# Performance work log

Hardware: AMD Instinct MI355X
Metric: run time of the kernel (lower is better)

## Reference

```python
import jax, jax.numpy as jnp
import numpy as np

NUM_BINS = 36
EPS = 1e-12
BASE_DROP, MIN_DROP, MAX_DROP = 0.3, 0.1, 0.6
SENSITIVITY, NORMAL_APE = 4.0, 0.78


def _hann(n):
    # torch.hann_window default (periodic=True): 0.5*(1 - cos(2*pi*k/N))
    return 0.5 - 0.5 * jnp.cos(2.0 * jnp.pi * jnp.arange(n, dtype=jnp.float32) / n)


def compute_ape(images):
    B, C, H, W = images.shape
    mean = jnp.array([0.485, 0.456, 0.406], dtype=images.dtype).reshape(1, 3, 1, 1)
    std = jnp.array([0.229, 0.224, 0.225], dtype=images.dtype).reshape(1, 3, 1, 1)
    wts = jnp.array([0.2989, 0.587, 0.114], dtype=images.dtype).reshape(1, 3, 1, 1)
    gray = ((images * std + mean) * wts).sum(axis=1)  # (B,H,W)
    gray = gray - gray.mean(axis=(1, 2), keepdims=True)
    gray = gray * (_hann(H)[:, None] * _hann(W)[None, :])
    P = jnp.abs(jnp.fft.fft2(gray)) ** 2
    P = jnp.fft.fftshift(P, axes=(1, 2))
    cy, cx = (H - 1) / 2.0, (W - 1) / 2.0
    yy = jnp.arange(H, dtype=jnp.float32)[:, None] - cy
    xx = jnp.arange(W, dtype=jnp.float32)[None, :] - cx
    r = jnp.sqrt(xx ** 2 + yy ** 2)
    theta = (jnp.arctan2(yy, xx) + 2 * jnp.pi) % (2 * jnp.pi)
    r_max = r.max()
    radial_mask = (r >= 0.05 * r_max) & (r <= 0.95 * r_max)
    bin_width = 2 * jnp.pi / NUM_BINS
    idx = jnp.clip((theta / bin_width).astype(jnp.int32), 0, NUM_BINS - 1)  # (H,W)
    # batched masked angular histogram: one segment_sum over B*NUM_BINS segments
    Pm = (P * radial_mask).reshape(B, -1)
    seg = (idx.reshape(-1)[None, :] + NUM_BINS * jnp.arange(B)[:, None]).reshape(-1)
    energy = jax.ops.segment_sum(Pm.reshape(-1), seg, num_segments=B * NUM_BINS)
    energy = energy.reshape(B, NUM_BINS)
    total = energy.sum(axis=1, keepdims=True)
    p = energy / (total + EPS)
    H_theta = -(p * jnp.log(p + EPS)).sum(axis=1)
    ape = jnp.clip(H_theta / np.log(NUM_BINS), 0.0, 1.0)
    return jnp.where(total[:, 0] <= EPS, 0.0, ape)


def ape_to_dropout_prob(ape):
    adj = jnp.tanh((NORMAL_APE - ape) * SENSITIVITY)
    drop = jnp.where(adj >= 0,
                     BASE_DROP + adj * (MAX_DROP - BASE_DROP),
                     BASE_DROP + adj * (BASE_DROP - MIN_DROP))
    return jnp.clip(drop, MIN_DROP, MAX_DROP)


def adaptive_dropout(x, probs, key):
    # per-sample dropout: mask ~ Bernoulli(1-p), scale by 1/(1-p+1e-8)
    p = probs[:, None, None]
    keep = jax.random.bernoulli(key, 1.0 - p, x.shape).astype(x.dtype)
    out = x * keep / (1.0 - p + 1e-8)
    return jnp.where(p > 0, out, x)


def setup_inputs() -> dict:
    key = jax.random.key(0)
    k1, k2, k3, k4 = jax.random.split(key, 4)
    B, N, D, Hf = 64, 256, 768, 768
    images = jax.random.uniform(k1, (B, 3, 448, 448), dtype=jnp.float32)
    x = jax.random.normal(k2, (B, N, D), dtype=jnp.float32)
    w1 = jax.random.normal(k3, (Hf, D), dtype=jnp.float32) * (1.0 / np.sqrt(D))
    w2 = jax.random.normal(k4, (D, Hf), dtype=jnp.float32) * (1.0 / np.sqrt(Hf))
    return {"images": images, "x": x, "w1": w1, "w2": w2}


def reference(images, x, w1, w2):
    ape = compute_ape(images)
    probs = jax.lax.stop_gradient(ape_to_dropout_prob(ape))  # torch casts to python float -> detached
    k0, k1, k2 = jax.random.split(jax.random.key(1), 3)
    h = adaptive_dropout(x, probs, k0)            # input dropout
    h = jnp.einsum('bnd,hd->bnh', h, w1)          # fc1 (bias=False)
    h = jax.nn.gelu(h, approximate=False)         # nn.GELU (exact erf)
    h = adaptive_dropout(h, probs, k1)
    y = jnp.einsum('bnh,dh->bnd', h, w2)          # fc2 (bias=False)
    y = adaptive_dropout(y, probs, k2)
    return y
```

## Files before the change

kernel.cpp:

```cpp
#include <hip/hip_runtime.h>
#include <stdint.h>
#include <math.h>

typedef __attribute__((ext_vector_type(8))) short short8;
typedef __attribute__((ext_vector_type(4))) float floatx4;

#define IMGN 448
#define HW   200704
#define NBATCH 64
#define NBINS 36

#define MFMA(a, b, c) __builtin_amdgcn_mfma_f32_16x16x32_bf16((a), (b), (c), 0, 0, 0)

#define WAITBAR8() asm volatile("s_waitcnt vmcnt(8)\ns_barrier" ::: "memory")
#define WAITBAR6() asm volatile("s_waitcnt vmcnt(6)\ns_barrier" ::: "memory")
#define WAITBAR4() asm volatile("s_waitcnt vmcnt(4)\ns_barrier" ::: "memory")
#define WAITBAR0() asm volatile("s_waitcnt vmcnt(0)\ns_barrier" ::: "memory")
#define ENDBAR()   asm volatile("s_waitcnt lgkmcnt(0)\ns_barrier" ::: "memory")

#define WS_WIN   0u
#define WS_BINS  4096u
#define WS_TS    24576u
#define WS_BIDX  32768u
#define WS_TW    1048576u
#define TWSZ     401408u
#define WS_W     4194304u
#define WSZ      1179648u
#define WS_REG1  16777216u
#define GSZ      25690112u
#define CBSZ     13762560u
#define XSZ      25165824u
#define WS_REG2  75497472u

__host__ __device__ __forceinline__ uint32_t rotl32(uint32_t v, int r) {
  return (v << r) | (v >> (32 - r));
}
__host__ __device__ __forceinline__ void tf2x32(uint32_t k0, uint32_t k1,
                                                uint32_t x0, uint32_t x1,
                                                uint32_t &o0, uint32_t &o1) {
  uint32_t k2 = k0 ^ k1 ^ 0x1BD11BDAu;
  uint32_t v0 = x0 + k0, v1 = x1 + k1;
#define TFR(r) { v0 += v1; v1 = rotl32(v1, r); v1 ^= v0; }
  TFR(13) TFR(15) TFR(26) TFR(6)   v0 += k1; v1 += k2 + 1u;
  TFR(17) TFR(29) TFR(16) TFR(24)  v0 += k2; v1 += k0 + 2u;
  TFR(13) TFR(15) TFR(26) TFR(6)   v0 += k0; v1 += k1 + 3u;
  TFR(17) TFR(29) TFR(16) TFR(24)  v0 += k1; v1 += k2 + 4u;
  TFR(13) TFR(15) TFR(26) TFR(6)   v0 += k2; v1 += k0 + 5u;
#undef TFR
  o0 = v0; o1 = v1;
}
__device__ __forceinline__ float tf_uniform(uint32_t k0, uint32_t k1, uint32_t idx) {
  uint32_t a, b;
  tf2x32(k0, k1, 0u, idx, a, b);
  uint32_t bits = a ^ b;
  return __uint_as_float((bits >> 9) | 0x3F800000u) - 1.0f;
}

__device__ __forceinline__ unsigned short bf16rne(float v) {
  unsigned u = __float_as_uint(v);
  return (unsigned short)((u + 0x7fffu + ((u >> 16) & 1u)) >> 16);
}
__device__ __forceinline__ void split2(float v, unsigned short &h, unsigned short &l) {
  h = bf16rne(v);
  float fh = __uint_as_float(((unsigned)h) << 16);
  l = bf16rne(v - fh);
}

__device__ __forceinline__ void gload16(const void *g, void *l) {
  __builtin_amdgcn_global_load_lds(
      (const __attribute__((address_space(1))) unsigned int *)g,
      (__attribute__((address_space(3))) unsigned int *)l, 16, 0, 0);
}

__global__ __launch_bounds__(256) void k_prep(float *__restrict__ win,
                                              double *__restrict__ bins,
                                              uint8_t *__restrict__ bidx) {
  int t = blockIdx.x * 256 + threadIdx.x;
  int a = t / IMGN, b = t % IMGN;
  double yy = (double)((a + 224) % IMGN) - 223.5;
  double xx = (double)((b + 224) % IMGN) - 223.5;
  double r2 = xx * xx + yy * yy;
  uint8_t idx = 255;
  if (r2 >= 249.76125 && r2 <= 90163.81125) {
    double th = atan2(yy, xx);
    if (th < 0.0) th += 6.283185307179586476925286766559;
    int i = (int)(th / 0.17453292519943295769236907684886);
    if (i > 35) i = 35;
    if (i < 0) i = 0;
    idx = (uint8_t)i;
  }
  bidx[t] = idx;
  if (t < IMGN) {
    double ang = 6.283185307179586476925286766559 * (double)t / 448.0;
    win[t] = (float)(0.5 - 0.5 * cos(ang));
  }
  if (t < NBATCH * NBINS) bins[t] = 0.0;
}

__global__ __launch_bounds__(256) void k_tw(short8 *__restrict__ tch, short8 *__restrict__ tcl,
                                            short8 *__restrict__ tsh, short8 *__restrict__ tsl) {
  int wid = blockIdx.x * 256 + threadIdx.x;
  int lane = wid & 63;
  int tmp = wid >> 6;
  int kb = tmp % 14, mb = tmp / 14;
  int m = mb * 16 + (lane & 15);
  int k0 = kb * 32 + (lane >> 4) * 8;
  short8 ch, cl, sh, sl;
#pragma unroll
  for (int e = 0; e < 8; ++e) {
    int mm = (m * (k0 + e)) % IMGN;
    double ang = -6.283185307179586476925286766559 * (double)mm / 448.0;
    float c = (float)cos(ang), s = (float)sin(ang);
    unsigned short h, l;
    split2(c, h, l); ch[e] = (short)h; cl[e] = (short)l;
    split2(s, h, l); sh[e] = (short)h; sl[e] = (short)l;
  }
  tch[wid] = ch; tcl[wid] = cl; tsh[wid] = sh; tsl[wid] = sl;
}

__global__ __launch_bounds__(256) void k_wconv(const float *__restrict__ w1, const float *__restrict__ w2,
                                               short8 *__restrict__ w1h, short8 *__restrict__ w1l,
                                               short8 *__restrict__ w2h, short8 *__restrict__ w2l) {
  int wid = blockIdx.x * 256 + threadIdx.x;
  const float *src = blockIdx.y ? w2 : w1;
  short8 *dh = blockIdx.y ? w2h : w1h;
  short8 *dl = blockIdx.y ? w2l : w1l;
  int lane = wid & 63;
  int tmp = wid >> 6;
  int kb = tmp % 24, nb = tmp / 24;
  int n = nb * 16 + (lane & 15);
  int k0 = kb * 32 + (lane >> 4) * 8;
  const float *p = src + (size_t)n * 768 + k0;
  short8 vh, vl;
#pragma unroll
  for (int e = 0; e < 8; ++e) {
    unsigned short h, l;
    split2(p[e], h, l);
    vh[e] = (short)h; vl[e] = (short)l;
  }
  dh[wid] = vh; dl[wid] = vl;
}

__global__ __launch_bounds__(256) void k_gprep(const float *__restrict__ img, const float *__restrict__ win,
                                               short8 *__restrict__ gh, short8 *__restrict__ gl) {
  int wid = blockIdx.x * 256 + threadIdx.x;
  int lane = wid & 63;
  int tmp = wid >> 6;
  int kb = tmp % 14, nb = tmp / 14;
  int n = nb * 16 + (lane & 15);
  int b = n / 448, y = n % 448;
  int x0 = kb * 32 + (lane >> 4) * 8;
  const float *p = img + (size_t)b * 3 * HW + y * IMGN + x0;
  float wy = win[y];
  short8 vh, vl;
#pragma unroll
  for (int e = 0; e < 8; ++e) {
    float r = p[e], g = p[HW + e], bl = p[2 * HW + e];
    float t0 = (r * 0.229f + 0.485f) * 0.2989f;
    float t1 = (g * 0.224f + 0.456f) * 0.587f;
    float t2 = (bl * 0.225f + 0.406f) * 0.114f;
    float v = ((t0 + t1) + t2) * wy * win[x0 + e];
    unsigned short h, l;
    split2(v, h, l);
    vh[e] = (short)h; vl[e] = (short)l;
  }
  gh[wid] = vh; gl[wid] = vl;
}

__global__ __launch_bounds__(256) void k_rows(const short8 *__restrict__ tch, const short8 *__restrict__ tcl,
                                              const short8 *__restrict__ tsh, const short8 *__restrict__ tsl,
                                              const short8 *__restrict__ gh, const short8 *__restrict__ gl,
                                              short8 *__restrict__ crh, short8 *__restrict__ crl,
                                              short8 *__restrict__ cih, short8 *__restrict__ cil) {
  __shared__ short8 S[2][512];
  int orig = blockIdx.x;
  int swz = (orig & 7) * 224 + (orig >> 3);
  int mtg = swz & 3, ntg = swz >> 2;
  int tid = threadIdx.x;
  int lane = tid & 63, w = tid >> 6;
  int g = lane >> 4, c = lane & 15;
  int mt = mtg * 4 + w;
  floatx4 s_c[4] = {}, s_s[4] = {};
  short8 aAc, aAcl, aAs, aAsl, aBc, aBcl, aBs, aBsl;

#define R_STAGE(buf, kb) { \
  _Pragma("unroll") for (int i = 0; i < 2; ++i) { \
    int ch = w * 2 + i; \
    const short8 *m0 = (ch >> 2) ? gl : gh; \
    int row = ntg * 4 + (ch & 3); \
    gload16(m0 + ((size_t)row * 14 + (kb)) * 64 + lane, (char *)&S[buf][0] + ch * 1024); } }
#define R_LOADA(p, kb) { int ao = (mt * 14 + (kb)) * 64 + lane; \
  p##c = tch[ao]; p##cl = tcl[ao]; p##s = tsh[ao]; p##sl = tsl[ao]; }
#define R_COMPUTE(buf, p) { const short8 *Sc = &S[buf][0]; \
  _Pragma("unroll") for (int nt = 0; nt < 4; ++nt) { \
    short8 bh = Sc[nt * 64 + lane]; \
    short8 bl = Sc[(4 + nt) * 64 + lane]; \
    s_c[nt] = MFMA(p##c, bh, s_c[nt]); \
    s_c[nt] = MFMA(p##c, bl, s_c[nt]); \
    s_c[nt] = MFMA(p##cl, bh, s_c[nt]); \
    s_s[nt] = MFMA(p##s, bh, s_s[nt]); \
    s_s[nt] = MFMA(p##s, bl, s_s[nt]); \
    s_s[nt] = MFMA(p##sl, bh, s_s[nt]); } }

  R_STAGE(0, 0); R_LOADA(aA, 0);
  for (int kb = 0; kb < 14; kb += 2) {
    R_STAGE(1, kb + 1); R_LOADA(aB, kb + 1);
    WAITBAR6();
    R_COMPUTE(0, aA);
    ENDBAR();
    if (kb < 12) { R_STAGE(0, kb + 2); R_LOADA(aA, kb + 2); WAITBAR6(); }
    else { WAITBAR0(); }
    R_COMPUTE(1, aB);
    ENDBAR();
  }
#pragma unroll
  for (int nt = 0; nt < 4; ++nt) {
    int nrow = (ntg * 4 + nt) * 16 + c;
    int b = nrow / 448, y = nrow % 448;
    int kb2 = y >> 5;
    int lofs = 16 * ((y & 31) >> 3);
    int e2 = y & 7;
#pragma unroll
    for (int r = 0; r < 4; ++r) {
      int v = mt * 16 + 4 * g + r;
      if (v < 240) {
        int n2 = b * 240 + v;
        size_t word = ((size_t)(n2 >> 4) * 14 + kb2) * 64 + (n2 & 15) + lofs;
        unsigned short h, l;
        split2(s_c[nt][r], h, l);
        ((unsigned short *)crh)[word * 8 + e2] = h;
        ((unsigned short *)crl)[word * 8 + e2] = l;
        split2(s_s[nt][r], h, l);
        ((unsigned short *)cih)[word * 8 + e2] = h;
        ((unsigned short *)cil)[word * 8 + e2] = l;
      }
    }
  }
}

__global__ __launch_bounds__(256) void k_cols(const short8 *__restrict__ tch, const short8 *__restrict__ tcl,
                                              const short8 *__restrict__ tsh, const short8 *__restrict__ tsl,
                                              const short8 *__restrict__ crh, const short8 *__restrict__ crl,
                                              const short8 *__restrict__ cih, const short8 *__restrict__ cil,
                                              const uint8_t *__restrict__ bidx, double *__restrict__ bins) {
  __shared__ short8 S[2][1024];
  __shared__ double lb[72];
  int orig = blockIdx.x;
  int swz = (orig & 7) * 210 + (orig >> 3);
  int mtg = swz % 7, ntg = swz / 7;
  int tid = threadIdx.x;
  if (tid < 72) lb[tid] = 0.0;
  int lane = tid & 63, w = tid >> 6;
  int g = lane >> 4, c = lane & 15;
  int mt = mtg * 4 + w;
  int nt0 = ntg * 4;
  floatx4 s_cc[4] = {}, s_sc[4] = {}, s_ss[4] = {}, s_cs[4] = {};
  short8 aAc, aAcl, aAs, aAsl, aBc, aBcl, aBs, aBsl;

#define C_STAGE(buf, kb) { \
  _Pragma("unroll") for (int i = 0; i < 4; ++i) { \
    int ch = w * 4 + i; int sel = ch >> 2; \
    const short8 *m0 = sel == 0 ? crh : sel == 1 ? crl : sel == 2 ? cih : cil; \
    int row = nt0 + (ch & 3); \
    gload16(m0 + ((size_t)row * 14 + (kb)) * 64 + lane, (char *)&S[buf][0] + ch * 1024); } }
#define C_LOADA(p, kb) { int ao = (mt * 14 + (kb)) * 64 + lane; \
  p##c = tch[ao]; p##cl = tcl[ao]; p##s = tsh[ao]; p##sl = tsl[ao]; }
#define C_COMPUTE(buf, p) { const short8 *Sc = &S[buf][0]; \
  _Pragma("unroll") for (int nt = 0; nt < 4; ++nt) { \
    short8 brh = Sc[nt * 64 + lane]; \
    short8 brl = Sc[(4 + nt) * 64 + lane]; \
    short8 bih = Sc[(8 + nt) * 64 + lane]; \
    short8 bil = Sc[(12 + nt) * 64 + lane]; \
    s_cc[nt] = MFMA(p##c, brh, s_cc[nt]); \
    s_cc[nt] = MFMA(p##c, brl, s_cc[nt]); \
    s_cc[nt] = MFMA(p##cl, brh, s_cc[nt]); \
    s_sc[nt] = MFMA(p##s, brh, s_sc[nt]); \
    s_sc[nt] = MFMA(p##s, brl, s_sc[nt]); \
    s_sc[nt] = MFMA(p##sl, brh, s_sc[nt]); \
    s_ss[nt] = MFMA(p##s, bih, s_ss[nt]); \
    s_ss[nt] = MFMA(p##s, bil, s_ss[nt]); \
    s_ss[nt] = MFMA(p##sl, bih, s_ss[nt]); \
    s_cs[nt] = MFMA(p##c, bih, s_cs[nt]); \
    s_cs[nt] = MFMA(p##c, bil, s_cs[nt]); \
    s_cs[nt] = MFMA(p##cl, bih, s_cs[nt]); } }

  C_STAGE(0, 0); C_LOADA(aA, 0);
  for (int kb = 0; kb < 14; kb += 2) {
    C_STAGE(1, kb + 1); C_LOADA(aB, kb + 1);
    WAITBAR8();
    C_COMPUTE(0, aA);
    ENDBAR();
    if (kb < 12) { C_STAGE(0, kb + 2); C_LOADA(aA, kb + 2); WAITBAR8(); }
    else { WAITBAR0(); }
    C_COMPUTE(1, aB);
    ENDBAR();
  }
  int base_b = (ntg * 64) / 240;
  int cb0 = -1, cb1 = -1, cb2 = -1, cb3 = -1;
  double cv0 = 0.0, cv1 = 0.0, cv2 = 0.0, cv3 = 0.0;
#define PUTBIN(slot_, val_)                                                    \
  { int _s = (slot_); double _v = (val_);                                      \
    if (_s == cb0) cv0 += _v;                                                  \
    else if (_s == cb1) cv1 += _v;                                             \
    else if (_s == cb2) cv2 += _v;                                             \
    else if (_s == cb3) cv3 += _v;                                             \
    else {                                                                     \
      if (cb3 >= 0) atomicAdd(&lb[cb3], cv3);                                  \
      cb3 = cb2; cv3 = cv2; cb2 = cb1; cv2 = cv1;                              \
      cb1 = cb0; cv1 = cv0; cb0 = _s; cv0 = _v;                                \
    } }
#pragma unroll
  for (int nt = 0; nt < 4; ++nt) {
    int n = (nt0 + nt) * 16 + c;
    int v = n % 240;
    int bloc = n / 240 - base_b;
    if (v < 225) {
#pragma unroll
      for (int r = 0; r < 4; ++r) {
        int u = mt * 16 + 4 * g + r;
        float frv = s_cc[nt][r] - s_ss[nt][r];
        float fiv = s_sc[nt][r] + s_cs[nt][r];
        double P = (double)frv * frv + (double)fiv * fiv;
        int i1 = bidx[u * IMGN + v];
        if (i1 < 36) PUTBIN(bloc * 36 + i1, P);
        if (v >= 1 && v <= 223) {
          int i2 = bidx[((IMGN - u) % IMGN) * IMGN + (IMGN - v)];
          if (i2 < 36) PUTBIN(bloc * 36 + i2, P);
        }
      }
    }
  }
  if (cb0 >= 0) atomicAdd(&lb[cb0], cv0);
  if (cb1 >= 0) atomicAdd(&lb[cb1], cv1);
  if (cb2 >= 0) atomicAdd(&lb[cb2], cv2);
  if (cb3 >= 0) atomicAdd(&lb[cb3], cv3);
#undef PUTBIN
  __syncthreads();
  if (tid < 72) {
    int bb = base_b + tid / 36;
    if (bb < NBATCH && lb[tid] != 0.0) atomicAdd(&bins[bb * NBINS + (tid % 36)], lb[tid]);
  }
}

__global__ void k_probs(const double *__restrict__ bins, float *__restrict__ ts) {
  int b = threadIdx.x;
  if (b >= NBATCH) return;
  double T = 0.0;
  for (int i = 0; i < NBINS; ++i) T += bins[b * NBINS + i];
  double H = 0.0;
  for (int i = 0; i < NBINS; ++i) {
    double p = bins[b * NBINS + i] / (T + 1e-12);
    H -= p * log(p + 1e-12);
  }
  double ape = H / 3.5835189384561099;
  if (ape > 1.0) ape = 1.0;
  if (ape < 0.0) ape = 0.0;
  if (T <= 1e-12) ape = 0.0;
  double adj = tanh((0.78 - ape) * 4.0);
  double drop = (adj >= 0.0) ? (0.3 + adj * 0.3) : (0.3 + adj * 0.2);
  if (drop < 0.1) drop = 0.1;
  if (drop > 0.6) drop = 0.6;
  float p32 = (float)drop;
  ts[b] = 1.0f - p32;
  ts[NBATCH + b] = 1.0f / (1.0f - p32 + 1e-8f);
}

__global__ __launch_bounds__(256) void k_dropfrag(const float *__restrict__ x, const float *__restrict__ ts,
                                                  short8 *__restrict__ xh, short8 *__restrict__ xl,
                                                  uint32_t k0, uint32_t k1) {
  int wid = blockIdx.x * 256 + threadIdx.x;
  int lane = wid & 63;
  int tmp = wid >> 6;
  int kb = tmp % 24, mb = tmp / 24;
  int m = mb * 16 + (lane & 15);
  int d0 = kb * 32 + (lane >> 4) * 8;
  int bi = m >> 8;
  float t = ts[bi], s = ts[NBATCH + bi];
  const float *p = x + (size_t)m * 768 + d0;
  short8 vh, vl;
#pragma unroll
  for (int e = 0; e < 8; ++e) {
    uint32_t idx = (uint32_t)m * 768u + (uint32_t)(d0 + e);
    float u = tf_uniform(k0, k1, idx);
    float v = (u < t) ? p[e] * s : 0.0f;
    unsigned short h, l;
    split2(v, h, l);
    vh[e] = (short)h; vl[e] = (short)l;
  }
  xh[wid] = vh; xl[wid] = vl;
}

template <int MODE>
__global__ __launch_bounds__(256) void k_mlp(const short8 *__restrict__ ah, const short8 *__restrict__ al,
                                             const short8 *__restrict__ bh, const short8 *__restrict__ bl,
                                             const float *__restrict__ ts, float *__restrict__ out,
                                             short8 *__restrict__ oh, short8 *__restrict__ ol,
                                             uint32_t k0, uint32_t k1) {
  __shared__ short8 S[2][512];
  int orig = blockIdx.x;
  int swz = (orig & 7) * 384 + (orig >> 3);
  int ntg = swz % 12, mtg = swz / 12;
  int tid = threadIdx.x;
  int lane = tid & 63, w = tid >> 6;
  int g = lane >> 4, c = lane & 15;
  int mt = mtg * 4 + w;
  int nt0 = ntg * 4;
  floatx4 acc[4] = {};
  short8 aAh, aAl, aBh, aBl;

#define M_STAGE(buf, kb) { \
  _Pragma("unroll") for (int i = 0; i < 2; ++i) { \
    int ch = w * 2 + i; \
    const short8 *m0 = (ch >> 2) ? bl : bh; \
    int row = nt0 + (ch & 3); \
    gload16(m0 + ((size_t)row * 24 + (kb)) * 64 + lane, (char *)&S[buf][0] + ch * 1024); } }
#define M_LOADA(p, kb) { int ao = (mt * 24 + (kb)) * 64 + lane; \
  p##h = ah[ao]; p##l = al[ao]; }
#define M_COMPUTE(buf, p) { const short8 *Sc = &S[buf][0]; \
  _Pragma("unroll") for (int nt = 0; nt < 4; ++nt) { \
    short8 b_h = Sc[nt * 64 + lane]; \
    short8 b_l = Sc[(4 + nt) * 64 + lane]; \
    acc[nt] = MFMA(p##h, b_h, acc[nt]); \
    acc[nt] = MFMA(p##h, b_l, acc[nt]); \
    acc[nt] = MFMA(p##l, b_h, acc[nt]); } }

  M_STAGE(0, 0); M_LOADA(aA, 0);
  for (int kb = 0; kb < 24; kb += 2) {
    M_STAGE(1, kb + 1); M_LOADA(aB, kb + 1);
    WAITBAR4();
    M_COMPUTE(0, aA);
    ENDBAR();
    if (kb < 22) { M_STAGE(0, kb + 2); M_LOADA(aA, kb + 2); WAITBAR4(); }
    else { WAITBAR0(); }
    M_COMPUTE(1, aB);
    ENDBAR();
  }
#pragma unroll
  for (int nt = 0; nt < 4; ++nt) {
    int n = (nt0 + nt) * 16 + c;
#pragma unroll
    for (int r = 0; r < 4; ++r) {
      int m = mt * 16 + 4 * g + r;
      float val = acc[nt][r];
      if (MODE == 1)
        val = 0.5f * val * (1.0f + erff(val * 0.70710678118654752440f));
      int bi = m >> 8;
      float t = ts[bi], s = ts[NBATCH + bi];
      uint32_t idx = (uint32_t)m * 768u + (uint32_t)n;
      float u = tf_uniform(k0, k1, idx);
      val = (u < t) ? val * s : 0.0f;
      if (MODE == 1) {
        unsigned short hh, hl;
        split2(val, hh, hl);
        int kb2 = n >> 5;
        int lane2 = (m & 15) + 16 * ((n & 31) >> 3);
        int e2 = n & 7;
        size_t word = ((size_t)(m >> 4) * 24 + kb2) * 64 + lane2;
        ((unsigned short *)oh)[word * 8 + e2] = hh;
        ((unsigned short *)ol)[word * 8 + e2] = hl;
      } else {
        out[(size_t)m * 768 + n] = val;
      }
    }
  }
}

extern "C" void kernel_launch(void *const *d_in, const int *in_sizes, int n_in,
                              void *d_out, int out_size, void *d_ws, size_t ws_size,
                              hipStream_t stream) {
  (void)in_sizes; (void)n_in; (void)out_size; (void)ws_size;
  const float *images = (const float *)d_in[0];
  const float *x  = (const float *)d_in[1];
  const float *w1 = (const float *)d_in[2];
  const float *w2 = (const float *)d_in[3];

  char *ws = (char *)d_ws;
  float   *win  = (float *)  (ws + WS_WIN);
  double  *bins = (double *) (ws + WS_BINS);
  float   *ts   = (float *)  (ws + WS_TS);
  uint8_t *bidx = (uint8_t *)(ws + WS_BIDX);
  short8  *tch  = (short8 *) (ws + WS_TW + 0 * TWSZ);
  short8  *tcl  = (short8 *) (ws + WS_TW + 1 * TWSZ);
  short8  *tsh  = (short8 *) (ws + WS_TW + 2 * TWSZ);
  short8  *tsl  = (short8 *) (ws + WS_TW + 3 * TWSZ);
  short8  *w1h  = (short8 *) (ws + WS_W + 0 * WSZ);
  short8  *w1l  = (short8 *) (ws + WS_W + 1 * WSZ);
  short8  *w2h  = (short8 *) (ws + WS_W + 2 * WSZ);
  short8  *w2l  = (short8 *) (ws + WS_W + 3 * WSZ);
  short8  *gh   = (short8 *) (ws + WS_REG1 + 0 * GSZ);
  short8  *gl   = (short8 *) (ws + WS_REG1 + 1 * GSZ);
  short8  *xh   = (short8 *) (ws + WS_REG1 + 0 * XSZ);
  short8  *xl   = (short8 *) (ws + WS_REG1 + 1 * XSZ);
  short8  *crh  = (short8 *) (ws + WS_REG2 + 0 * CBSZ);
  short8  *crl  = (short8 *) (ws + WS_REG2 + 1 * CBSZ);
  short8  *cih  = (short8 *) (ws + WS_REG2 + 2 * CBSZ);
  short8  *cil  = (short8 *) (ws + WS_REG2 + 3 * CBSZ);
  short8  *hh_  = (short8 *) (ws + WS_REG2 + 0 * XSZ);
  short8  *hl_  = (short8 *) (ws + WS_REG2 + 1 * XSZ);
  float   *yout = (float *)d_out;

  uint32_t keys[6];
  tf2x32(0u, 1u, 0u, 0u, keys[0], keys[1]);
  tf2x32(0u, 1u, 0u, 1u, keys[2], keys[3]);
  tf2x32(0u, 1u, 0u, 2u, keys[4], keys[5]);

  k_prep<<<784, 256, 0, stream>>>(win, bins, bidx);
  k_tw<<<98, 256, 0, stream>>>(tch, tcl, tsh, tsl);
  k_wconv<<<dim3(288, 2), 256, 0, stream>>>(w1, w2, w1h, w1l, w2h, w2l);
  k_gprep<<<6272, 256, 0, stream>>>(images, win, gh, gl);
  k_rows<<<1792, 256, 0, stream>>>(tch, tcl, tsh, tsl, gh, gl, crh, crl, cih, cil);
  k_cols<<<1680, 256, 0, stream>>>(tch, tcl, tsh, tsl, crh, crl, cih, cil, bidx, bins);
  k_probs<<<1, 64, 0, stream>>>(bins, ts);
  k_dropfrag<<<6144, 256, 0, stream>>>(x, ts, xh, xl, keys[0], keys[1]);
  k_mlp<1><<<3072, 256, 0, stream>>>(xh, xl, w1h, w1l, ts, yout, hh_, hl_, keys[2], keys[3]);
  k_mlp<2><<<3072, 256, 0, stream>>>(hh_, hl_, w2h, w2l, ts, yout, hh_, hl_, keys[4], keys[5]);
}
```

Baseline: 400.9 us.

## Drop LDS double-buffering; widen k_rows M-tile, triple K-step in MLP

k_rows now has each wave compute two M-tiles, which halves the grid and reuses each LDS B tile across twice the MFMA work. Its double-buffered pipeline is replaced by a single buffer with __syncthreads. k_mlp stages three K-blocks per iteration into a larger single LDS buffer and drops the manual vmcnt pipelining, so there are fewer barriers per unit of work. The trade-off is that load/compute overlap inside a block is lost, k_rows needs more registers (lower occupancy), and the larger LDS footprint in k_mlp may limit resident blocks.

```diff
diff --git a/kernel.cpp b/kernel.cpp
--- a/kernel.cpp
+++ b/kernel.cpp
@@ -13,8 +13,6 @@
 #define MFMA(a, b, c) __builtin_amdgcn_mfma_f32_16x16x32_bf16((a), (b), (c), 0, 0, 0)
 
 #define WAITBAR8() asm volatile("s_waitcnt vmcnt(8)\ns_barrier" ::: "memory")
-#define WAITBAR6() asm volatile("s_waitcnt vmcnt(6)\ns_barrier" ::: "memory")
-#define WAITBAR4() asm volatile("s_waitcnt vmcnt(4)\ns_barrier" ::: "memory")
 #define WAITBAR0() asm volatile("s_waitcnt vmcnt(0)\ns_barrier" ::: "memory")
 #define ENDBAR()   asm volatile("s_waitcnt lgkmcnt(0)\ns_barrier" ::: "memory")
 
@@ -172,70 +170,74 @@
                                               const short8 *__restrict__ gh, const short8 *__restrict__ gl,
                                               short8 *__restrict__ crh, short8 *__restrict__ crl,
                                               short8 *__restrict__ cih, short8 *__restrict__ cil) {
-  __shared__ short8 S[2][512];
+  __shared__ short8 S[512];
   int orig = blockIdx.x;
-  int swz = (orig & 7) * 224 + (orig >> 3);
-  int mtg = swz & 3, ntg = swz >> 2;
+  int swz = (orig & 7) * 112 + (orig >> 3);
+  int mtg = swz & 1, ntg = swz >> 1;
   int tid = threadIdx.x;
   int lane = tid & 63, w = tid >> 6;
   int g = lane >> 4, c = lane & 15;
-  int mt = mtg * 4 + w;
-  floatx4 s_c[4] = {}, s_s[4] = {};
-  short8 aAc, aAcl, aAs, aAsl, aBc, aBcl, aBs, aBsl;
-
-#define R_STAGE(buf, kb) { \
-  _Pragma("unroll") for (int i = 0; i < 2; ++i) { \
-    int ch = w * 2 + i; \
-    const short8 *m0 = (ch >> 2) ? gl : gh; \
-    int row = ntg * 4 + (ch & 3); \
-    gload16(m0 + ((size_t)row * 14 + (kb)) * 64 + lane, (char *)&S[buf][0] + ch * 1024); } }
-#define R_LOADA(p, kb) { int ao = (mt * 14 + (kb)) * 64 + lane; \
-  p##c = tch[ao]; p##cl = tcl[ao]; p##s = tsh[ao]; p##sl = tsl[ao]; }
-#define R_COMPUTE(buf, p) { const short8 *Sc = &S[buf][0]; \
-  _Pragma("unroll") for (int nt = 0; nt < 4; ++nt) { \
-    short8 bh = Sc[nt * 64 + lane]; \
-    short8 bl = Sc[(4 + nt) * 64 + lane]; \
-    s_c[nt] = MFMA(p##c, bh, s_c[nt]); \
-    s_c[nt] = MFMA(p##c, bl, s_c[nt]); \
-    s_c[nt] = MFMA(p##cl, bh, s_c[nt]); \
-    s_s[nt] = MFMA(p##s, bh, s_s[nt]); \
-    s_s[nt] = MFMA(p##s, bl, s_s[nt]); \
-    s_s[nt] = MFMA(p##sl, bh, s_s[nt]); } }
-
-  R_STAGE(0, 0); R_LOADA(aA, 0);
-  for (int kb = 0; kb < 14; kb += 2) {
-    R_STAGE(1, kb + 1); R_LOADA(aB, kb + 1);
-    WAITBAR6();
-    R_COMPUTE(0, aA);
-    ENDBAR();
-    if (kb < 12) { R_STAGE(0, kb + 2); R_LOADA(aA, kb + 2); WAITBAR6(); }
-    else { WAITBAR0(); }
-    R_COMPUTE(1, aB);
-    ENDBAR();
-  }
-#pragma unroll
-  for (int nt = 0; nt < 4; ++nt) {
-    int nrow = (ntg * 4 + nt) * 16 + c;
-    int b = nrow / 448, y = nrow % 448;
-    int kb2 = y >> 5;
-    int lofs = 16 * ((y & 31) >> 3);
-    int e2 = y & 7;
-#pragma unroll
-    for (int r = 0; r < 4; ++r) {
-      int v = mt * 16 + 4 * g + r;
-      if (v < 240) {
-        int n2 = b * 240 + v;
-        size_t word = ((size_t)(n2 >> 4) * 14 + kb2) * 64 + (n2 & 15) + lofs;
-        unsigned short h, l;
-        split2(s_c[nt][r], h, l);
-        ((unsigned short *)crh)[word * 8 + e2] = h;
-        ((unsigned short *)crl)[word * 8 + e2] = l;
-        split2(s_s[nt][r], h, l);
-        ((unsigned short *)cih)[word * 8 + e2] = h;
-        ((unsigned short *)cil)[word * 8 + e2] = l;
-      }
+  int mt0 = mtg * 8 + w * 2;
+  floatx4 sc0[4] = {}, ss0[4] = {}, sc1[4] = {}, ss1[4] = {};
+  for (int kb = 0; kb < 14; ++kb) {
+#pragma unroll
+    for (int i = 0; i < 2; ++i) {
+      int ch = w * 2 + i;
+      const short8 *m0 = (ch >> 2) ? gl : gh;
+      int row = ntg * 4 + (ch & 3);
+      gload16(m0 + ((size_t)row * 14 + kb) * 64 + lane, (char *)S + ch * 1024);
     }
-  }
+    int ao0 = (mt0 * 14 + kb) * 64 + lane;
+    int ao1 = ao0 + 14 * 64;
+    short8 c0 = tch[ao0], l0 = tcl[ao0], s0 = tsh[ao0], z0 = tsl[ao0];
+    short8 c1 = tch[ao1], l1 = tcl[ao1], s1 = tsh[ao1], z1 = tsl[ao1];
+    __syncthreads();
+#pragma unroll
+    for (int nt = 0; nt < 4; ++nt) {
+      short8 bh = S[nt * 64 + lane];
+      short8 bl = S[(4 + nt) * 64 + lane];
+      sc0[nt] = MFMA(c0, bh, sc0[nt]);
+      sc0[nt] = MFMA(c0, bl, sc0[nt]);
+      sc0[nt] = MFMA(l0, bh, sc0[nt]);
+      ss0[nt] = MFMA(s0, bh, ss0[nt]);
+      ss0[nt] = MFMA(s0, bl, ss0[nt]);
+      ss0[nt] = MFMA(z0, bh, ss0[nt]);
+      sc1[nt] = MFMA(c1, bh, sc1[nt]);
+      sc1[nt] = MFMA(c1, bl, sc1[nt]);
+      sc1[nt] = MFMA(l1, bh, sc1[nt]);
+      ss1[nt] = MFMA(s1, bh, ss1[nt]);
+      ss1[nt] = MFMA(s1, bl, ss1[nt]);
+      ss1[nt] = MFMA(z1, bh, ss1[nt]);
+    }
+    __syncthreads();
+  }
+#define R_EPI(SC, SS, MT)                                                      \
+  {                                                                            \
+    _Pragma("unroll") for (int nt = 0; nt < 4; ++nt) {                         \
+      int nrow = (ntg * 4 + nt) * 16 + c;                                      \
+      int b = nrow / 448, y = nrow % 448;                                      \
+      int kb2 = y >> 5;                                                        \
+      int lofs = 16 * ((y & 31) >> 3);                                         \
+      int e2 = y & 7;                                                          \
+      _Pragma("unroll") for (int r = 0; r < 4; ++r) {                          \
+        int v = (MT) * 16 + 4 * g + r;                                         \
+        if (v < 240) {                                                         \
+          int n2 = b * 240 + v;                                                \
+          size_t word = ((size_t)(n2 >> 4) * 14 + kb2) * 64 + (n2 & 15) + lofs;\
+          unsigned short h, l;                                                 \
+          split2(SC[nt][r], h, l);                                             \
+          ((unsigned short *)crh)[word * 8 + e2] = h;                          \
+          ((unsigned short *)crl)[word * 8 + e2] = l;                          \
+          split2(SS[nt][r], h, l);                                             \
+          ((unsigned short *)cih)[word * 8 + e2] = h;                          \
+          ((unsigned short *)cil)[word * 8 + e2] = l;                          \
+        }                                                                      \
+      }                                                                        \
+    }                                                                          \
+  }
+  R_EPI(sc0, ss0, mt0)
+  R_EPI(sc1, ss1, mt0 + 1)
+#undef R_EPI
 }
 
 __global__ __launch_bounds__(256) void k_cols(const short8 *__restrict__ tch, const short8 *__restrict__ tcl,
@@ -396,7 +398,7 @@
                                              const float *__restrict__ ts, float *__restrict__ out,
                                              short8 *__restrict__ oh, short8 *__restrict__ ol,
                                              uint32_t k0, uint32_t k1) {
-  __shared__ short8 S[2][512];
+  __shared__ short8 S[1536];
   int orig = blockIdx.x;
   int swz = (orig & 7) * 384 + (orig >> 3);
   int ntg = swz % 12, mtg = swz / 12;
@@ -406,34 +408,37 @@
   int mt = mtg * 4 + w;
   int nt0 = ntg * 4;
   floatx4 acc[4] = {};
-  short8 aAh, aAl, aBh, aBl;
-
-#define M_STAGE(buf, kb) { \
-  _Pragma("unroll") for (int i = 0; i < 2; ++i) { \
-    int ch = w * 2 + i; \
-    const short8 *m0 = (ch >> 2) ? bl : bh; \
-    int row = nt0 + (ch & 3); \
-    gload16(m0 + ((size_t)row * 24 + (kb)) * 64 + lane, (char *)&S[buf][0] + ch * 1024); } }
-#define M_LOADA(p, kb) { int ao = (mt * 24 + (kb)) * 64 + lane; \
-  p##h = ah[ao]; p##l = al[ao]; }
-#define M_COMPUTE(buf, p) { const short8 *Sc = &S[buf][0]; \
-  _Pragma("unroll") for (int nt = 0; nt < 4; ++nt) { \
-    short8 b_h = Sc[nt * 64 + lane]; \
-    short8 b_l = Sc[(4 + nt) * 64 + lane]; \
-    acc[nt] = MFMA(p##h, b_h, acc[nt]); \
-    acc[nt] = MFMA(p##h, b_l, acc[nt]); \
-    acc[nt] = MFMA(p##l, b_h, acc[nt]); } }
-
-  M_STAGE(0, 0); M_LOADA(aA, 0);
-  for (int kb = 0; kb < 24; kb += 2) {
-    M_STAGE(1, kb + 1); M_LOADA(aB, kb + 1);
-    WAITBAR4();
-    M_COMPUTE(0, aA);
-    ENDBAR();
-    if (kb < 22) { M_STAGE(0, kb + 2); M_LOADA(aA, kb + 2); WAITBAR4(); }
-    else { WAITBAR0(); }
-    M_COMPUTE(1, aB);
-    ENDBAR();
+  for (int kb = 0; kb < 24; kb += 3) {
+#pragma unroll
+    for (int i = 0; i < 6; ++i) {
+      int ch = w * 6 + i;
+      int kk = ch >> 3, rem = ch & 7;
+      const short8 *m0 = (rem >> 2) ? bl : bh;
+      int row = nt0 + (rem & 3);
+      gload16(m0 + ((size_t)row * 24 + kb + kk) * 64 + lane, (char *)S + ch * 1024);
+    }
+    int ao = (mt * 24 + kb) * 64 + lane;
+    short8 h0 = ah[ao],       l0 = al[ao];
+    short8 h1 = ah[ao + 64],  l1 = al[ao + 64];
+    short8 h2 = ah[ao + 128], l2 = al[ao + 128];
+    __syncthreads();
+#pragma unroll
+    for (int nt = 0; nt < 4; ++nt) {
+      short8 b_h, b_l;
+      b_h = S[nt * 64 + lane];        b_l = S[(4 + nt) * 64 + lane];
+      acc[nt] = MFMA(h0, b_h, acc[nt]);
+      acc[nt] = MFMA(h0, b_l, acc[nt]);
+      acc[nt] = MFMA(l0, b_h, acc[nt]);
+      b_h = S[(8 + nt) * 64 + lane];  b_l = S[(12 + nt) * 64 + lane];
+      acc[nt] = MFMA(h1, b_h, acc[nt]);
+      acc[nt] = MFMA(h1, b_l, acc[nt]);
+      acc[nt] = MFMA(l1, b_h, acc[nt]);
+      b_h = S[(16 + nt) * 64 + lane]; b_l = S[(20 + nt) * 64 + lane];
+      acc[nt] = MFMA(h2, b_h, acc[nt]);
+      acc[nt] = MFMA(h2, b_l, acc[nt]);
+      acc[nt] = MFMA(l2, b_h, acc[nt]);
+    }
+    __syncthreads();
   }
 #pragma unroll
   for (int nt = 0; nt < 4; ++nt) {
@@ -508,7 +513,7 @@
   k_tw<<<98, 256, 0, stream>>>(tch, tcl, tsh, tsl);
   k_wconv<<<dim3(288, 2), 256, 0, stream>>>(w1, w2, w1h, w1l, w2h, w2l);
   k_gprep<<<6272, 256, 0, stream>>>(images, win, gh, gl);
-  k_rows<<<1792, 256, 0, stream>>>(tch, tcl, tsh, tsl, gh, gl, crh, crl, cih, cil);
+  k_rows<<<896, 256, 0, stream>>>(tch, tcl, tsh, tsl, gh, gl, crh, crl, cih, cil);
   k_cols<<<1680, 256, 0, stream>>>(tch, tcl, tsh, tsl, crh, crl, cih, cil, bidx, bins);
   k_probs<<<1, 64, 0, stream>>>(bins, ts);
   k_dropfrag<<<6144, 256, 0, stream>>>(x, ts, xh, xl, keys[0], keys[1]);
```

Measured after the change: 409.7 us. +2.2%, slower.
